# Kernel tuning notes

Measured on AMD Instinct MI355X. Metric: run time of the kernel, lower is better.

## Reference

```python
import jax, jax.numpy as jnp
import numpy as np

B, N, C = 8, 1024, 768
H = 12
HD = C // H
STAGES = 3
MLP_H = 4 * C
EPS = 1e-5


def _layernorm(x, w, b):
    mu = jnp.mean(x, axis=-1, keepdims=True)
    var = jnp.mean(jnp.square(x - mu), axis=-1, keepdims=True)
    return (x - mu) * jax.lax.rsqrt(var + EPS) * w + b


def setup_inputs() -> dict:
    key = jax.random.key(0)
    ks = jax.random.split(key, 16)
    s = 0.02
    return {
        "x": jax.random.normal(ks[0], (B, N, C), dtype=jnp.float32),
        # stacked per-stage attention params (torch Linear layout: [out, in])
        "qkv_w": jax.random.normal(ks[1], (STAGES, 3 * C, C), dtype=jnp.float32) * s,
        "proj_w": jax.random.normal(ks[2], (STAGES, C, C), dtype=jnp.float32) * s,
        "proj_b": jnp.zeros((STAGES, C), dtype=jnp.float32),
        "ln1_w": jnp.ones((C,), dtype=jnp.float32),
        "ln1_b": jnp.zeros((C,), dtype=jnp.float32),
        "ln2_w": jnp.ones((C,), dtype=jnp.float32),
        "ln2_b": jnp.zeros((C,), dtype=jnp.float32),
        "mlp_w1": jax.random.normal(ks[3], (MLP_H, C), dtype=jnp.float32) * s,
        "mlp_b1": jnp.zeros((MLP_H,), dtype=jnp.float32),
        "mlp_w2": jax.random.normal(ks[4], (C, MLP_H), dtype=jnp.float32) * s,
        "mlp_b2": jnp.zeros((C,), dtype=jnp.float32),
        "focus_w": jnp.ones((STAGES,), dtype=jnp.float32),
    }


def reference(x, qkv_w, proj_w, proj_b, ln1_w, ln1_b, ln2_w, ln2_b,
              mlp_w1, mlp_b1, mlp_w2, mlp_b2, focus_w):
    scale = HD ** -0.5
    h = _layernorm(x, ln1_w, ln1_b)  # shared norm1(x) input to all stages
    attn_out = jnp.zeros_like(x)
    for i in range(STAGES):
        qkv = jnp.einsum('bnc,oc->bno', h, qkv_w[i])  # [B,N,3C], no bias (qkv_bias=False)
        qkv = qkv.reshape(B, N, 3, H, HD).transpose(2, 0, 3, 1, 4)  # [3,B,H,N,HD]
        q, k, v = qkv[0], qkv[1], qkv[2]
        attn = jax.nn.softmax(jnp.einsum('bhnd,bhmd->bhnm', q, k) * scale, axis=-1)
        o = jnp.einsum('bhnm,bhmd->bhnd', attn, v)  # [B,H,N,HD]
        o = o.transpose(0, 2, 1, 3).reshape(B, N, C)
        o = jnp.einsum('bnc,oc->bno', o, proj_w[i]) + proj_b[i]
        attn_out = attn_out + focus_w[i] * o
    x = x + attn_out
    h2 = _layernorm(x, ln2_w, ln2_b)
    h2 = jax.nn.gelu(jnp.einsum('bnc,hc->bnh', h2, mlp_w1) + mlp_b1, approximate=False)
    mlp_out = jnp.einsum('bnh,ch->bnc', h2, mlp_w2) + mlp_b2
    return x + mlp_out
```

## Files before the change

### kernel.cpp

```cpp
#include <hip/hip_runtime.h>
#include <hip/hip_bf16.h>
#include <math.h>

#define B_    8
#define N_    1024
#define C_    768
#define H_    12
#define HD_   64
#define MLPH_ 3072
#define M_ROWS 8192
#define QKV3  6912
#define PK    2304

typedef float  f32x4  __attribute__((ext_vector_type(4)));
typedef __bf16 bf16x8 __attribute__((ext_vector_type(8)));

__device__ __forceinline__ f32x4 mfma16(bf16x8 a, bf16x8 b, f32x4 c) {
    return __builtin_amdgcn_mfma_f32_16x16x32_bf16(a, b, c, 0, 0, 0);
}

__global__ __launch_bounds__(256) void cast_f32_bf16(const float* __restrict__ in,
                                                     __bf16* __restrict__ out, int n) {
    int i = blockIdx.x * 256 + threadIdx.x;
    if (i < n) out[i] = (__bf16)in[i];
}

__global__ __launch_bounds__(256) void prep_proj_w(const float* __restrict__ pw,
                                                   const float* __restrict__ focus,
                                                   __bf16* __restrict__ out) {
    int i = blockIdx.x * 256 + threadIdx.x;
    int c = i % C_;
    int s = (i / C_) % 3;
    int o = i / PK;
    out[i] = (__bf16)(focus[s] * pw[((size_t)s * C_ + o) * C_ + c]);
}

__global__ __launch_bounds__(256) void ln_to_bf16(const float* __restrict__ x,
                                                  const float* __restrict__ g,
                                                  const float* __restrict__ bta,
                                                  __bf16* __restrict__ out) {
    int row = blockIdx.x;
    const float* xr = x + (size_t)row * C_;
    int t = threadIdx.x;
    float v0 = xr[t], v1 = xr[t + 256], v2 = xr[t + 512];
    float s  = v0 + v1 + v2;
    float s2 = v0 * v0 + v1 * v1 + v2 * v2;
#pragma unroll
    for (int m = 1; m < 64; m <<= 1) { s += __shfl_xor(s, m); s2 += __shfl_xor(s2, m); }
    __shared__ float red[8];
    int w = t >> 6, lane = t & 63;
    if (lane == 0) { red[w] = s; red[4 + w] = s2; }
    __syncthreads();
    s  = red[0] + red[1] + red[2] + red[3];
    s2 = red[4] + red[5] + red[6] + red[7];
    float mu   = s * (1.f / C_);
    float var  = s2 * (1.f / C_) - mu * mu;
    float rstd = rsqrtf(var + 1e-5f);
    __bf16* orow = out + (size_t)row * C_;
    orow[t]       = (__bf16)((v0 - mu) * rstd * g[t]       + bta[t]);
    orow[t + 256] = (__bf16)((v1 - mu) * rstd * g[t + 256] + bta[t + 256]);
    orow[t + 512] = (__bf16)((v2 - mu) * rstd * g[t + 512] + bta[t + 512]);
}

template <int MODE>
__global__ __launch_bounds__(256) void gemm_bt(
    const __bf16* __restrict__ A, const __bf16* __restrict__ W,
    int M, int N, int K,
    __bf16* __restrict__ obf, float* __restrict__ of32,
    const float* __restrict__ resid, const float* __restrict__ bias,
    const float* __restrict__ focus_p)
{
    __shared__ __bf16 As[128][40];
    __shared__ __bf16 Bs[128][40];

    const int t    = threadIdx.x;
    const int lane = t & 63;
    const int w    = t >> 6;
    const int wr   = w >> 1, wc = w & 1;
    const int m0   = blockIdx.y * 128, n0 = blockIdx.x * 128;
    const int lo   = lane & 15;
    const int lk8  = (lane >> 4) * 8;

    const int r0 = t >> 2;
    const int cb = (t & 3) * 8;

    f32x4 acc[4][4] = {};

    int4 ra0, ra1, rb0, rb1;
    auto load_tile = [&](int k0) {
        ra0 = *(const int4*)&A[(size_t)(m0 + r0)      * K + k0 + cb];
        ra1 = *(const int4*)&A[(size_t)(m0 + r0 + 64) * K + k0 + cb];
        rb0 = *(const int4*)&W[(size_t)(n0 + r0)      * K + k0 + cb];
        rb1 = *(const int4*)&W[(size_t)(n0 + r0 + 64) * K + k0 + cb];
    };
    load_tile(0);

    for (int k0 = 0; k0 < K; k0 += 32) {
        __syncthreads();
        *(int4*)&As[r0][cb]      = ra0;
        *(int4*)&As[r0 + 64][cb] = ra1;
        *(int4*)&Bs[r0][cb]      = rb0;
        *(int4*)&Bs[r0 + 64][cb] = rb1;
        __syncthreads();
        if (k0 + 32 < K) load_tile(k0 + 32);

        bf16x8 af[4], bfr[4];
#pragma unroll
        for (int mi = 0; mi < 4; mi++) af[mi]  = *(const bf16x8*)&As[wr * 64 + mi * 16 + lo][lk8];
#pragma unroll
        for (int ni = 0; ni < 4; ni++) bfr[ni] = *(const bf16x8*)&Bs[wc * 64 + ni * 16 + lo][lk8];
#pragma unroll
        for (int mi = 0; mi < 4; mi++)
#pragma unroll
            for (int ni = 0; ni < 4; ni++)
                acc[mi][ni] = mfma16(af[mi], bfr[ni], acc[mi][ni]);
    }

    float f0 = 0.f, f1 = 0.f, f2 = 0.f;
    if (MODE == 1) { f0 = focus_p[0]; f1 = focus_p[1]; f2 = focus_p[2]; }

#pragma unroll
    for (int mi = 0; mi < 4; mi++) {
#pragma unroll
        for (int ni = 0; ni < 4; ni++) {
            int col = n0 + wc * 64 + ni * 16 + lo;
#pragma unroll
            for (int r = 0; r < 4; r++) {
                int row = m0 + wr * 64 + mi * 16 + (lane >> 4) * 4 + r;
                size_t o = (size_t)row * N + col;
                float v = acc[mi][ni][r];
                if (MODE == 0) {
                    obf[o] = (__bf16)v;
                } else if (MODE == 1) {
                    float be = f0 * bias[col] + f1 * bias[col + C_] + f2 * bias[col + 2 * C_];
                    of32[o] = resid[o] + v + be;
                } else if (MODE == 2) {
                    float u = v + bias[col];
                    float ge = 0.5f * u * (1.0f + erff(u * 0.70710678118654752f));
                    obf[o] = (__bf16)ge;
                } else {
                    of32[o] = resid[o] + v + bias[col];
                }
            }
        }
    }
}

__global__ __launch_bounds__(256) void attn_kernel(const __bf16* __restrict__ qkv,
                                                   __bf16* __restrict__ obuf) {
    const int bid  = blockIdx.x;
    const int idx  = bid >> 3;
    const int grp  = (bid & 7) * 36 + (idx >> 3);
    const int qt   = idx & 7;
    const int s    = grp / 96;
    const int rem  = grp % 96;
    const int b    = rem / 12;
    const int h    = rem % 12;
    const int q0   = qt * 128;

    const int t = threadIdx.x, lane = t & 63, w = t >> 6;
    const int lo = lane & 15, hi = lane >> 4;

    __shared__ __bf16 Ks[64][72];
    __shared__ __bf16 Vt[64][72];
    __shared__ __bf16 Ps[128][72];

    const size_t rs = QKV3;
    const __bf16* qb = qkv + (size_t)b * N_ * rs + (size_t)s * PK + h * HD_;
    const __bf16* kb = qb + C_;
    const __bf16* vb = qb + 2 * C_;

    bf16x8 aq[2][2];
#pragma unroll
    for (int mi = 0; mi < 2; mi++) {
        const __bf16* p = qb + (size_t)(q0 + w * 32 + mi * 16 + lo) * rs + hi * 8;
        aq[mi][0] = *(const bf16x8*)p;
        aq[mi][1] = *(const bf16x8*)(p + 32);
    }

    bf16x8 ones;
#pragma unroll
    for (int j = 0; j < 8; j++) ones[j] = (__bf16)1.0f;

    f32x4 oacc[2][4] = {};
    f32x4 lsum[2] = {};

    int4 kreg[2]; bf16x8 vreg[2];
    auto load_tile = [&](int k0) {
#pragma unroll
        for (int p = 0; p < 2; p++) {
            int id = p * 256 + t;
            int kr = id >> 3, d0 = (id & 7) * 8;
            kreg[p] = *(const int4*)(kb + (size_t)(k0 + kr) * rs + d0);
            int kr2 = id & 63, d2 = (id >> 6) * 8;
            vreg[p] = *(const bf16x8*)(vb + (size_t)(k0 + kr2) * rs + d2);
        }
    };
    load_tile(0);

    const float cexp = 0.18033688011112042f;

    for (int kt = 0; kt < 16; kt++) {
        __syncthreads();
#pragma unroll
        for (int p = 0; p < 2; p++) {
            int id = p * 256 + t;
            int kr = id >> 3, d0 = (id & 7) * 8;
            *(int4*)&Ks[kr][d0] = kreg[p];
            int kr2 = id & 63, d2 = (id >> 6) * 8;
#pragma unroll
            for (int j = 0; j < 8; j++) Vt[d2 + j][kr2] = vreg[p][j];
        }
        __syncthreads();
        if (kt < 15) load_tile((kt + 1) * 64);

        bf16x8 kfr[4][2];
#pragma unroll
        for (int kf = 0; kf < 4; kf++) {
            kfr[kf][0] = *(const bf16x8*)&Ks[kf * 16 + lo][hi * 8];
            kfr[kf][1] = *(const bf16x8*)&Ks[kf * 16 + lo][32 + hi * 8];
        }
        f32x4 sacc[2][4] = {};
#pragma unroll
        for (int mi = 0; mi < 2; mi++)
#pragma unroll
            for (int kf = 0; kf < 4; kf++) {
                sacc[mi][kf] = mfma16(aq[mi][0], kfr[kf][0], sacc[mi][kf]);
                sacc[mi][kf] = mfma16(aq[mi][1], kfr[kf][1], sacc[mi][kf]);
            }

#pragma unroll
        for (int mi = 0; mi < 2; mi++)
#pragma unroll
            for (int kf = 0; kf < 4; kf++)
#pragma unroll
                for (int r = 0; r < 4; r++) {
                    float pv = exp2f(sacc[mi][kf][r] * cexp);
                    Ps[w * 32 + mi * 16 + hi * 4 + r][kf * 16 + lo] = (__bf16)pv;
                }

        bf16x8 pa[2][2], vfr[4][2];
#pragma unroll
        for (int mi = 0; mi < 2; mi++) {
            pa[mi][0] = *(const bf16x8*)&Ps[w * 32 + mi * 16 + lo][hi * 8];
            pa[mi][1] = *(const bf16x8*)&Ps[w * 32 + mi * 16 + lo][32 + hi * 8];
        }
#pragma unroll
        for (int df = 0; df < 4; df++) {
            vfr[df][0] = *(const bf16x8*)&Vt[df * 16 + lo][hi * 8];
            vfr[df][1] = *(const bf16x8*)&Vt[df * 16 + lo][32 + hi * 8];
        }
#pragma unroll
        for (int mi = 0; mi < 2; mi++) {
#pragma unroll
            for (int df = 0; df < 4; df++) {
                oacc[mi][df] = mfma16(pa[mi][0], vfr[df][0], oacc[mi][df]);
                oacc[mi][df] = mfma16(pa[mi][1], vfr[df][1], oacc[mi][df]);
            }
            lsum[mi] = mfma16(pa[mi][0], ones, lsum[mi]);
            lsum[mi] = mfma16(pa[mi][1], ones, lsum[mi]);
        }
    }

#pragma unroll
    for (int mi = 0; mi < 2; mi++)
#pragma unroll
        for (int r = 0; r < 4; r++) {
            float il = 1.0f / lsum[mi][r];
#pragma unroll
            for (int df = 0; df < 4; df++)
                Ps[w * 32 + mi * 16 + hi * 4 + r][df * 16 + lo] = (__bf16)(oacc[mi][df][r] * il);
        }
    __syncthreads();
    {
        int row = t >> 1, half = t & 1;
        __bf16* orow = obuf + ((size_t)b * N_ + q0 + row) * PK + (size_t)s * C_ + h * HD_ + half * 32;
#pragma unroll
        for (int j = 0; j < 4; j++)
            *(int4*)(orow + j * 8) = *(const int4*)&Ps[row][half * 32 + j * 8];
    }
}

extern "C" void kernel_launch(void* const* d_in, const int* in_sizes, int n_in,
                              void* d_out, int out_size, void* d_ws, size_t ws_size,
                              hipStream_t stream) {
    const float* x      = (const float*)d_in[0];
    const float* qkv_w  = (const float*)d_in[1];
    const float* proj_w = (const float*)d_in[2];
    const float* proj_b = (const float*)d_in[3];
    const float* ln1_w  = (const float*)d_in[4];
    const float* ln1_b  = (const float*)d_in[5];
    const float* ln2_w  = (const float*)d_in[6];
    const float* ln2_b  = (const float*)d_in[7];
    const float* mlp_w1 = (const float*)d_in[8];
    const float* mlp_b1 = (const float*)d_in[9];
    const float* mlp_w2 = (const float*)d_in[10];
    const float* mlp_b2 = (const float*)d_in[11];
    const float* focus  = (const float*)d_in[12];
    float* out = (float*)d_out;

    char* ws = (char*)d_ws;
    size_t off = 0;
    auto alloc = [&](size_t bytes) {
        char* p = ws + off;
        off += (bytes + 255) & ~(size_t)255;
        return p;
    };
    __bf16* h1   = (__bf16*)alloc((size_t)M_ROWS * C_ * 2);
    __bf16* qkvb = (__bf16*)alloc((size_t)M_ROWS * QKV3 * 2);
    __bf16* ob   = (__bf16*)alloc((size_t)M_ROWS * PK * 2);
    float*  x1   = (float*) alloc((size_t)M_ROWS * C_ * 4);
    __bf16* wq   = (__bf16*)alloc((size_t)QKV3 * C_ * 2);
    __bf16* wp   = (__bf16*)alloc((size_t)C_ * PK * 2);
    __bf16* w1   = (__bf16*)alloc((size_t)MLPH_ * C_ * 2);
    __bf16* w2   = (__bf16*)alloc((size_t)C_ * MLPH_ * 2);
    if (off > ws_size) return;
    __bf16* h2  = h1;
    __bf16* hid = qkvb;

    const int nq = QKV3 * C_;
    const int np = C_ * PK;
    const int n1 = MLPH_ * C_;
    cast_f32_bf16<<<(nq + 255) / 256, 256, 0, stream>>>(qkv_w, wq, nq);
    prep_proj_w<<<(np + 255) / 256, 256, 0, stream>>>(proj_w, focus, wp);
    cast_f32_bf16<<<(n1 + 255) / 256, 256, 0, stream>>>(mlp_w1, w1, n1);
    cast_f32_bf16<<<(n1 + 255) / 256, 256, 0, stream>>>(mlp_w2, w2, n1);

    ln_to_bf16<<<M_ROWS, 256, 0, stream>>>(x, ln1_w, ln1_b, h1);

    gemm_bt<0><<<dim3(QKV3 / 128, M_ROWS / 128), 256, 0, stream>>>(
        h1, wq, M_ROWS, QKV3, C_, qkvb, nullptr, nullptr, nullptr, nullptr);

    attn_kernel<<<3 * B_ * H_ * (N_ / 128), 256, 0, stream>>>(qkvb, ob);

    gemm_bt<1><<<dim3(C_ / 128, M_ROWS / 128), 256, 0, stream>>>(
        ob, wp, M_ROWS, C_, PK, nullptr, x1, x, proj_b, focus);

    ln_to_bf16<<<M_ROWS, 256, 0, stream>>>(x1, ln2_w, ln2_b, h2);

    gemm_bt<2><<<dim3(MLPH_ / 128, M_ROWS / 128), 256, 0, stream>>>(
        h2, w1, M_ROWS, MLPH_, C_, hid, nullptr, nullptr, mlp_b1, nullptr);
    gemm_bt<3><<<dim3(C_ / 128, M_ROWS / 128), 256, 0, stream>>>(
        hid, w2, M_ROWS, C_, MLPH_, nullptr, out, x1, mlp_b2, nullptr);
}
```

Measured before the change: 560.0 us.

## Rewrite attention inner loop with 32x32 MFMA and register-resident P

The attention kernel moves from 16x16x32 to 32x32x16 bf16 MFMA and computes S transposed (K as the A operand), so the exponentiated probabilities can be repacked in registers with permlane32_swap instead of round-tripping through the Ps shared buffer. K and V tiles are stored in XOR-swizzled flat LDS layouts, with V transposed via DPP lane swaps. The row sum is accumulated in scalar adds rather than extra MFMAs against a ones vector. Output is written straight from the accumulators after normalization, using scattered 2-byte stores instead of staged vector stores. This cuts LDS traffic and MFMA count but adds permute work and less coalesced output writes.

```diff
diff --git a/kernel.cpp b/kernel.cpp
--- a/kernel.cpp
+++ b/kernel.cpp
@@ -12,11 +12,22 @@
 #define QKV3  6912
 #define PK    2304
 
-typedef float  f32x4  __attribute__((ext_vector_type(4)));
-typedef __bf16 bf16x8 __attribute__((ext_vector_type(8)));
+typedef float  f32x4   __attribute__((ext_vector_type(4)));
+typedef float  f32x16  __attribute__((ext_vector_type(16)));
+typedef __bf16 bf16x8  __attribute__((ext_vector_type(8)));
 
 __device__ __forceinline__ f32x4 mfma16(bf16x8 a, bf16x8 b, f32x4 c) {
     return __builtin_amdgcn_mfma_f32_16x16x32_bf16(a, b, c, 0, 0, 0);
+}
+__device__ __forceinline__ f32x16 mfma32(bf16x8 a, bf16x8 b, f32x16 c) {
+    return __builtin_amdgcn_mfma_f32_32x32x16_bf16(a, b, c, 0, 0, 0);
+}
+
+__device__ __forceinline__ unsigned packbf(float a, float b) {
+    __bf16 x = (__bf16)a, y = (__bf16)b;
+    union { __bf16 h; unsigned short u; } ux, uy;
+    ux.h = x; uy.h = y;
+    return (unsigned)ux.u | ((unsigned)uy.u << 16);
 }
 
 __global__ __launch_bounds__(256) void cast_f32_bf16(const float* __restrict__ in,
@@ -159,41 +170,34 @@
     const int q0   = qt * 128;
 
     const int t = threadIdx.x, lane = t & 63, w = t >> 6;
-    const int lo = lane & 15, hi = lane >> 4;
-
-    __shared__ __bf16 Ks[64][72];
-    __shared__ __bf16 Vt[64][72];
-    __shared__ __bf16 Ps[128][72];
+    const int l31 = lane & 31, hi1 = lane >> 5;
+
+    __shared__ __bf16 Kf[4096];
+    __shared__ __bf16 Vf[4096];
+    __shared__ float  Lsm[128];
 
     const size_t rs = QKV3;
     const __bf16* qb = qkv + (size_t)b * N_ * rs + (size_t)s * PK + h * HD_;
     const __bf16* kb = qb + C_;
     const __bf16* vb = qb + 2 * C_;
 
-    bf16x8 aq[2][2];
-#pragma unroll
-    for (int mi = 0; mi < 2; mi++) {
-        const __bf16* p = qb + (size_t)(q0 + w * 32 + mi * 16 + lo) * rs + hi * 8;
-        aq[mi][0] = *(const bf16x8*)p;
-        aq[mi][1] = *(const bf16x8*)(p + 32);
-    }
-
-    bf16x8 ones;
-#pragma unroll
-    for (int j = 0; j < 8; j++) ones[j] = (__bf16)1.0f;
-
-    f32x4 oacc[2][4] = {};
-    f32x4 lsum[2] = {};
-
-    int4 kreg[2]; bf16x8 vreg[2];
+    bf16x8 aq[4];
+#pragma unroll
+    for (int dk = 0; dk < 4; dk++)
+        aq[dk] = *(const bf16x8*)(qb + (size_t)(q0 + w * 32 + l31) * rs + dk * 16 + hi1 * 8);
+
+    f32x16 oacc[2] = {};
+    float lsum = 0.f;
+
+    int4 kreg[2]; uint4 vreg[2];
     auto load_tile = [&](int k0) {
 #pragma unroll
         for (int p = 0; p < 2; p++) {
             int id = p * 256 + t;
             int kr = id >> 3, d0 = (id & 7) * 8;
             kreg[p] = *(const int4*)(kb + (size_t)(k0 + kr) * rs + d0);
-            int kr2 = id & 63, d2 = (id >> 6) * 8;
-            vreg[p] = *(const bf16x8*)(vb + (size_t)(k0 + kr2) * rs + d2);
+            int kr2 = id & 63, d2 = ((id >> 6) * 8);
+            vreg[p] = *(const uint4*)(vb + (size_t)(k0 + kr2) * rs + d2);
         }
     };
     load_tile(0);
@@ -205,80 +209,104 @@
 #pragma unroll
         for (int p = 0; p < 2; p++) {
             int id = p * 256 + t;
-            int kr = id >> 3, d0 = (id & 7) * 8;
-            *(int4*)&Ks[kr][d0] = kreg[p];
-            int kr2 = id & 63, d2 = (id >> 6) * 8;
-#pragma unroll
-            for (int j = 0; j < 8; j++) Vt[d2 + j][kr2] = vreg[p][j];
+            int chunk = (id & 7) * 64 + (id >> 3);
+            int c = chunk ^ (id & 7);
+            *(int4*)&Kf[c * 8] = kreg[p];
+        }
+        {
+            int k8 = lane >> 3, par = lane & 1, koff = lane & 6;
+#pragma unroll
+            for (int p = 0; p < 2; p++) {
+                int d2 = ((p * 256 + t) >> 6) * 8;
+#pragma unroll
+                for (int i = 0; i < 4; i++) {
+                    unsigned mw = vreg[p][i];
+                    unsigned pw = (unsigned)__builtin_amdgcn_mov_dpp((int)mw, 0xB1, 0xF, 0xF, true);
+                    unsigned out = par ? ((pw >> 16) | (mw & 0xFFFF0000u))
+                                       : ((mw & 0xFFFFu) | (pw << 16));
+                    int d = d2 + 2 * i + par;
+                    int chunk = k8 * 64 + d;
+                    int c = chunk ^ k8;
+                    *(unsigned*)&Vf[c * 8 + koff] = out;
+                }
+            }
         }
         __syncthreads();
         if (kt < 15) load_tile((kt + 1) * 64);
 
-        bf16x8 kfr[4][2];
-#pragma unroll
-        for (int kf = 0; kf < 4; kf++) {
-            kfr[kf][0] = *(const bf16x8*)&Ks[kf * 16 + lo][hi * 8];
-            kfr[kf][1] = *(const bf16x8*)&Ks[kf * 16 + lo][32 + hi * 8];
-        }
-        f32x4 sacc[2][4] = {};
-#pragma unroll
-        for (int mi = 0; mi < 2; mi++)
-#pragma unroll
-            for (int kf = 0; kf < 4; kf++) {
-                sacc[mi][kf] = mfma16(aq[mi][0], kfr[kf][0], sacc[mi][kf]);
-                sacc[mi][kf] = mfma16(aq[mi][1], kfr[kf][1], sacc[mi][kf]);
-            }
-
-#pragma unroll
-        for (int mi = 0; mi < 2; mi++)
-#pragma unroll
-            for (int kf = 0; kf < 4; kf++)
-#pragma unroll
-                for (int r = 0; r < 4; r++) {
-                    float pv = exp2f(sacc[mi][kf][r] * cexp);
-                    Ps[w * 32 + mi * 16 + hi * 4 + r][kf * 16 + lo] = (__bf16)pv;
+        f32x16 sacc[2] = {};
+#pragma unroll
+        for (int ks = 0; ks < 2; ks++)
+#pragma unroll
+            for (int dk = 0; dk < 4; dk++) {
+                int d8 = dk * 2 + hi1;
+                int c = (d8 * 64 + ks * 32 + l31) ^ d8;
+                bf16x8 kf = *(const bf16x8*)&Kf[c * 8];
+                sacc[ks] = mfma32(kf, aq[dk], sacc[ks]);
+            }
+
+#pragma unroll
+        for (int ks = 0; ks < 2; ks++) {
+            float pe[16];
+#pragma unroll
+            for (int r = 0; r < 16; r++) {
+                pe[r] = exp2f(sacc[ks][r] * cexp);
+                lsum += pe[r];
+            }
+            unsigned pk[8];
+#pragma unroll
+            for (int i = 0; i < 8; i++) pk[i] = packbf(pe[2 * i], pe[2 * i + 1]);
+
+            unsigned a0 = pk[0], a2 = pk[2], a1 = pk[1], a3 = pk[3];
+            {
+                auto r0 = __builtin_amdgcn_permlane32_swap((int)a0, (int)a2, false, false);
+                a0 = (unsigned)r0[0]; a2 = (unsigned)r0[1];
+                auto r1 = __builtin_amdgcn_permlane32_swap((int)a1, (int)a3, false, false);
+                a1 = (unsigned)r1[0]; a3 = (unsigned)r1[1];
+            }
+            unsigned b0 = pk[4], b2 = pk[6], b1 = pk[5], b3 = pk[7];
+            {
+                auto r0 = __builtin_amdgcn_permlane32_swap((int)b0, (int)b2, false, false);
+                b0 = (unsigned)r0[0]; b2 = (unsigned)r0[1];
+                auto r1 = __builtin_amdgcn_permlane32_swap((int)b1, (int)b3, false, false);
+                b1 = (unsigned)r1[0]; b3 = (unsigned)r1[1];
+            }
+            union { unsigned u[4]; bf16x8 v; } fr0, fr1;
+            fr0.u[0] = a0; fr0.u[1] = a1; fr0.u[2] = a2; fr0.u[3] = a3;
+            fr1.u[0] = b0; fr1.u[1] = b1; fr1.u[2] = b2; fr1.u[3] = b3;
+
+#pragma unroll
+            for (int f = 0; f < 2; f++) {
+                bf16x8 pa = f ? fr1.v : fr0.v;
+#pragma unroll
+                for (int dh = 0; dh < 2; dh++) {
+                    int k8 = ks * 4 + f * 2 + hi1;
+                    int c = (k8 * 64 + dh * 32 + l31) ^ k8;
+                    bf16x8 vf = *(const bf16x8*)&Vf[c * 8];
+                    oacc[dh] = mfma32(pa, vf, oacc[dh]);
                 }
-
-        bf16x8 pa[2][2], vfr[4][2];
-#pragma unroll
-        for (int mi = 0; mi < 2; mi++) {
-            pa[mi][0] = *(const bf16x8*)&Ps[w * 32 + mi * 16 + lo][hi * 8];
-            pa[mi][1] = *(const bf16x8*)&Ps[w * 32 + mi * 16 + lo][32 + hi * 8];
-        }
-#pragma unroll
-        for (int df = 0; df < 4; df++) {
-            vfr[df][0] = *(const bf16x8*)&Vt[df * 16 + lo][hi * 8];
-            vfr[df][1] = *(const bf16x8*)&Vt[df * 16 + lo][32 + hi * 8];
-        }
-#pragma unroll
-        for (int mi = 0; mi < 2; mi++) {
-#pragma unroll
-            for (int df = 0; df < 4; df++) {
-                oacc[mi][df] = mfma16(pa[mi][0], vfr[df][0], oacc[mi][df]);
-                oacc[mi][df] = mfma16(pa[mi][1], vfr[df][1], oacc[mi][df]);
-            }
-            lsum[mi] = mfma16(pa[mi][0], ones, lsum[mi]);
-            lsum[mi] = mfma16(pa[mi][1], ones, lsum[mi]);
+            }
         }
     }
 
-#pragma unroll
-    for (int mi = 0; mi < 2; mi++)
-#pragma unroll
-        for (int r = 0; r < 4; r++) {
-            float il = 1.0f / lsum[mi][r];
-#pragma unroll
-            for (int df = 0; df < 4; df++)
-                Ps[w * 32 + mi * 16 + hi * 4 + r][df * 16 + lo] = (__bf16)(oacc[mi][df][r] * il);
-        }
-    __syncthreads();
-    {
-        int row = t >> 1, half = t & 1;
-        __bf16* orow = obuf + ((size_t)b * N_ + q0 + row) * PK + (size_t)s * C_ + h * HD_ + half * 32;
-#pragma unroll
-        for (int j = 0; j < 4; j++)
-            *(int4*)(orow + j * 8) = *(const int4*)&Ps[row][half * 32 + j * 8];
-    }
+    float ls2 = lsum + __shfl_xor(lsum, 32);
+    if (lane < 32) Lsm[w * 32 + lane] = ls2;
+    f32x4 Ls[4];
+#pragma unroll
+    for (int g = 0; g < 4; g++)
+        Ls[g] = *(const f32x4*)&Lsm[w * 32 + 8 * g + 4 * hi1];
+
+    __bf16* obase = obuf + ((size_t)b * N_ + q0 + w * 32) * PK + (size_t)s * C_ + h * HD_ + l31;
+#pragma unroll
+    for (int g = 0; g < 4; g++)
+#pragma unroll
+        for (int i = 0; i < 4; i++) {
+            float inv = 1.0f / Ls[g][i];
+            int q_local = i + 8 * g + 4 * hi1;
+            __bf16* orow = obase + (size_t)q_local * PK;
+            orow[0]  = (__bf16)(oacc[0][4 * g + i] * inv);
+            orow[32] = (__bf16)(oacc[1][4 * g + i] * inv);
+        }
 }
 
 extern "C" void kernel_launch(void* const* d_in, const int* in_sizes, int n_in,
```

New measurement: 528.2 us. 1.06x faster.
